# Kernel optimization log

Measured on AMD Instinct MI355X. Metric: run time of the kernel, lower is better.

## Reference

```python
import jax, jax.numpy as jnp
from jax import lax
import numpy as np
import math

D = 96   # d_model
H = 4    # num_heads (d_k = d_v = D per head, per the source)
K = 7    # depthwise kernel size
L = 4    # num conv layers


def _pos_encoding(seq_len, d):
    # Faithful to the source's (nonstandard) exponents: sin uses 2*i/d, cos uses 2*(i+1)/d
    pos = np.arange(seq_len, dtype=np.float32)[:, None]
    i = np.arange(0, d, 2, dtype=np.float32)
    pe = np.zeros((seq_len, d), dtype=np.float32)
    pe[:, 0::2] = np.sin(pos / 10000.0 ** (2.0 * i / d))
    pe[:, 1::2] = np.cos(pos / 10000.0 ** (2.0 * (i + 1.0) / d))
    return jnp.asarray(pe)


def _layernorm(x, g, b, eps=1e-5):
    m = jnp.mean(x, axis=-1, keepdims=True)
    v = jnp.mean((x - m) ** 2, axis=-1, keepdims=True)
    return (x - m) / jnp.sqrt(v + eps) * g + b


def setup_inputs() -> dict:
    key = jax.random.key(0)
    ks = jax.random.split(key, 10)
    B, S = 128, 384

    def xavier(k, shape, fan_in, fan_out):
        bound = math.sqrt(6.0 / (fan_in + fan_out))
        return jax.random.uniform(k, shape, jnp.float32, -bound, bound)

    return {
        "input": jax.random.normal(ks[0], (B, S, D), jnp.float32),
        "mask": jnp.zeros((B, S), dtype=bool),
        "conv_dw": jax.random.normal(ks[1], (L, D, 1, K), jnp.float32) * 0.05,
        "conv_dw_b": jnp.zeros((L, D), jnp.float32),
        "conv_pw": jax.random.normal(ks[2], (L, D, D, 1), jnp.float32) * 0.05,
        "conv_pw_b": jnp.zeros((L, D), jnp.float32),
        "WQ": xavier(ks[3], (H, D, D), D, D),
        "WK": xavier(ks[4], (H, D, D), D, D),
        "WV": xavier(ks[5], (H, D, D), D, D),
        "WO": xavier(ks[6], (H * D, D), H * D, D),
        "ffn_w1": jax.random.normal(ks[7], (D, D // 2), jnp.float32) * 0.1,
        "ffn_b1": jnp.zeros((D // 2,), jnp.float32),
        "ffn_w2": jax.random.normal(ks[8], (D // 2, D), jnp.float32) * 0.1,
        "ffn_b2": jnp.zeros((D,), jnp.float32),
        "ln_g": jnp.ones((L + 2, D), jnp.float32),
        "ln_b": jnp.zeros((L + 2, D), jnp.float32),
    }


def reference(input, mask, conv_dw, conv_dw_b, conv_pw, conv_pw_b,
              WQ, WK, WV, WO, ffn_w1, ffn_b1, ffn_w2, ffn_b2, ln_g, ln_b):
    B, S, _ = input.shape
    dn = ("NCH", "OIH", "NCH")

    # positional encoding (eval mode: all dropout is identity)
    x = input * jnp.float32(math.sqrt(D)) + _pos_encoding(S, D)[None]

    # conv blocks: LN -> depthwise conv -> pointwise conv -> relu -> residual
    for i in range(L):
        h = _layernorm(x, ln_g[i], ln_b[i])
        h = jnp.transpose(h, (0, 2, 1))  # [B, C, S]
        h = lax.conv_general_dilated(h, conv_dw[i], (1,), "SAME",
                                     feature_group_count=D, dimension_numbers=dn)
        h = h + conv_dw_b[i][None, :, None]
        h = lax.conv_general_dilated(h, conv_pw[i], (1,), "SAME", dimension_numbers=dn)
        h = jax.nn.relu(h + conv_pw_b[i][None, :, None])
        x = x + jnp.transpose(h, (0, 2, 1))

    # multi-head attention with per-head full-width projections (d_k = D)
    h = _layernorm(x, ln_g[L], ln_b[L])
    Q = jnp.einsum("bsd,hde->hbse", h, WQ)
    Kh = jnp.einsum("bsd,hde->hbse", h, WK)
    V = jnp.einsum("bsd,hde->hbse", h, WV)
    # source divides scores by temperature = 1/sqrt(d_k) => multiply by sqrt(D)
    scores = jnp.einsum("hbqe,hbke->hbqk", Q, Kh) * jnp.float32(math.sqrt(D))
    # mask is viewed [B, S, 1]: masks query rows, broadcast over keys
    scores = jnp.where(mask[None, :, :, None], -jnp.inf, scores)
    attn = jax.nn.softmax(scores, axis=-1)
    ctx = jnp.einsum("hbqk,hbke->hbqe", attn, V)
    cat = jnp.transpose(ctx, (1, 2, 0, 3)).reshape(B, S, H * D)
    x = x + cat @ WO

    # feed-forward: Linear -> sigmoid -> Linear, residual
    h2 = _layernorm(x, ln_g[L + 1], ln_b[L + 1])
    ff = jax.nn.sigmoid(h2 @ ffn_w1 + ffn_b1) @ ffn_w2 + ffn_b2
    return x + ff
```

## Files before the change

### kernel.cpp

```cpp
#include <hip/hip_runtime.h>
#include <math.h>


constexpr int B = 128;
constexpr int S = 384;
constexpr int D = 96;
constexpr int H = 4;
constexpr int KW = 7;
constexpr int L = 4;
constexpr int ROWS = B * S;
constexpr long long NTOT = (long long)ROWS * D;
constexpr float SQRTD = 9.797958971132712f;

typedef _Float16 f16x8 __attribute__((ext_vector_type(8)));
typedef float f32x4 __attribute__((ext_vector_type(4)));
typedef unsigned short us;
typedef unsigned short us8 __attribute__((ext_vector_type(8)));

__device__ __forceinline__ us f2h(float f) {
    _Float16 h = (_Float16)f;
    return __builtin_bit_cast(us, h);
}
__device__ __forceinline__ f16x8 ldh(const us* p) {
    return *reinterpret_cast<const f16x8*>(p);
}

__global__ void pe_kernel(float* __restrict__ pe) {
    int idx = blockIdx.x * 256 + threadIdx.x;
    if (idx >= S * D) return;
    int s = idx / D, c = idx - s * D;
    int j = c >> 1;
    float expo = (c & 1) ? (4.0f * j + 2.0f) / 96.0f : (4.0f * j) / 96.0f;
    float freq = expf(-expo * logf(10000.0f));
    float ang = (float)s * freq;
    pe[idx] = (c & 1) ? cosf(ang) : sinf(ang);
}

__global__ void prep_w(const float* __restrict__ WQ, const float* __restrict__ WK,
                       const float* __restrict__ cpw, const float* __restrict__ w1,
                       const float* __restrict__ w2,
                       us* __restrict__ wqS, us* __restrict__ wkT, us* __restrict__ pw16,
                       us* __restrict__ w1T, us* __restrict__ w2Tp) {
    int idx = blockIdx.x * 256 + threadIdx.x;
    if (idx >= H * D * D) return;
    int h = idx / (D * D), rem = idx - h * (D * D);
    int d = rem / D, e = rem - d * D;
    int n = e >> 4, lmod = e & 15, kk = d >> 5, ldiv = (d >> 3) & 3, j = d & 7;
    wqS[(size_t)(((h * 6 + n) * 3 + kk) * 64 + ldiv * 16 + lmod) * 8 + j] = f2h(WQ[idx] * SQRTD);
    wkT[(size_t)h * D * D + e * D + d] = f2h(WK[idx]);
    pw16[idx] = f2h(cpw[idx]);
    if (idx < 48 * 96) {
        int m = idx / 96, c = idx - m * 96;
        w1T[idx] = f2h(w1[c * 48 + m]);
    }
    if (idx < 96 * 64) {
        int o = idx / 64, m = idx - o * 64;
        w2Tp[idx] = (m < 48) ? f2h(w2[m * 96 + o]) : (us)0;
    }
}

__global__ void prep_wvo(const float* __restrict__ WV, const float* __restrict__ WO,
                         us* __restrict__ wvoT) {
    int blk = blockIdx.x;
    int h = blk / 6, ot = blk - h * 6;
    int tid = threadIdx.x;
    const float* wv = WV + (size_t)h * D * D;
    const float* wo = WO + (size_t)h * D * D;
    for (int i = tid; i < 16 * 96; i += 256) {
        int o = ot * 16 + i / 96, d = i - (i / 96) * 96;
        float acc = 0.f;
        for (int e = 0; e < 96; e++) acc += wv[d * 96 + e] * wo[e * 96 + o];
        wvoT[(size_t)h * D * D + o * 96 + d] = f2h(acc);
    }
}

__global__ void embed_ln(const float* __restrict__ in, const float* __restrict__ pe,
                         const float* __restrict__ gln, const float* __restrict__ bln,
                         float* __restrict__ x, us* __restrict__ lnout) {
    int wave = threadIdx.x >> 6;
    int lane = threadIdx.x & 63;
    int row = blockIdx.x * 4 + wave;
    if (row >= ROWS) return;
    int s = row % S;
    size_t ro = (size_t)row * D;
    float v0 = in[ro + lane] * SQRTD + pe[s * 96 + lane];
    float v1 = (lane < 32) ? in[ro + 64 + lane] * SQRTD + pe[s * 96 + 64 + lane] : 0.f;
    x[ro + lane] = v0;
    if (lane < 32) x[ro + 64 + lane] = v1;
    float sm = v0 + v1, q = v0 * v0 + v1 * v1;
    for (int off = 32; off > 0; off >>= 1) {
        sm += __shfl_xor(sm, off);
        q += __shfl_xor(q, off);
    }
    float mean = sm * (1.0f / D);
    float var = q * (1.0f / D) - mean * mean;
    float rstd = rsqrtf(var + 1e-5f);
    lnout[ro + lane] = f2h((v0 - mean) * rstd * gln[lane] + bln[lane]);
    if (lane < 32)
        lnout[ro + 64 + lane] = f2h((v1 - mean) * rstd * gln[lane + 64] + bln[lane + 64]);
}

__global__ void conv2(const float* __restrict__ xin, const us* __restrict__ lnin,
                      float* __restrict__ xout, us* __restrict__ lnout,
                      const float* __restrict__ dwW, const float* __restrict__ dwB,
                      const us* __restrict__ pwW, const float* __restrict__ pwb,
                      const float* __restrict__ gnext, const float* __restrict__ bnext) {
    __shared__ us dwb_s[64 * 104];
    __shared__ float lw[96 * 8];
    int tid = threadIdx.x;
    int wave = tid >> 6, lane = tid & 63;
    int r0 = blockIdx.x * 64;
    int b = r0 / S, s0 = r0 % S;

    for (int i = tid; i < 96 * KW; i += 256) lw[(i / KW) * 8 + (i % KW)] = dwW[i];
    __syncthreads();

    for (int u = tid; u < 768; u += 256) {
        int j = u / 12, c0 = (u - (u / 12) * 12) * 8;
        float acc[8];
        #pragma unroll
        for (int j2 = 0; j2 < 8; j2++) acc[j2] = dwB[c0 + j2];
        #pragma unroll
        for (int k = 0; k < KW; k++) {
            int ss = s0 + j + k - 3;
            if ((unsigned)ss < (unsigned)S) {
                f16x8 v = ldh(lnin + ((size_t)b * S + ss) * 96 + c0);
                #pragma unroll
                for (int j2 = 0; j2 < 8; j2++) acc[j2] += (float)v[j2] * lw[(c0 + j2) * 8 + k];
            }
        }
        us8 o;
        #pragma unroll
        for (int j2 = 0; j2 < 8; j2++) o[j2] = f2h(acc[j2]);
        *reinterpret_cast<us8*>(&dwb_s[j * 104 + c0]) = o;
    }
    __syncthreads();

    int lmod = lane & 15, ldiv = lane >> 4, m0 = wave * 16;
    f32x4 acc[6] = {};
    #pragma unroll
    for (int kk = 0; kk < 3; kk++) {
        f16x8 af = ldh(&dwb_s[(m0 + lmod) * 104 + kk * 32 + ldiv * 8]);
        #pragma unroll
        for (int n = 0; n < 6; n++) {
            f16x8 bf = ldh(pwW + (size_t)(n * 16 + lmod) * 96 + kk * 32 + ldiv * 8);
            acc[n] = __builtin_amdgcn_mfma_f32_16x16x32_f16(af, bf, acc[n], 0, 0, 0);
        }
    }

    float gv[6], bv2[6], pb[6];
    #pragma unroll
    for (int n = 0; n < 6; n++) {
        int o = n * 16 + lmod;
        gv[n] = gnext[o];
        bv2[n] = bnext[o];
        pb[n] = pwb[o];
    }
    #pragma unroll
    for (int n = 0; n < 6; n++) {
        #pragma unroll
        for (int r = 0; r < 4; r++) {
            size_t row = (size_t)r0 + m0 + ldiv * 4 + r;
            acc[n][r] = xin[row * 96 + n * 16 + lmod] + fmaxf(acc[n][r] + pb[n], 0.f);
        }
    }
    #pragma unroll
    for (int r = 0; r < 4; r++) {
        float sm = 0.f, qq = 0.f;
        #pragma unroll
        for (int n = 0; n < 6; n++) {
            sm += acc[n][r];
            qq += acc[n][r] * acc[n][r];
        }
        #pragma unroll
        for (int st = 1; st <= 8; st <<= 1) {
            sm += __shfl_xor(sm, st);
            qq += __shfl_xor(qq, st);
        }
        float mean = sm * (1.0f / D);
        float var = qq * (1.0f / D) - mean * mean;
        float rstd = rsqrtf(var + 1e-5f);
        size_t row = (size_t)r0 + m0 + ldiv * 4 + r;
        #pragma unroll
        for (int n = 0; n < 6; n++) {
            int o = n * 16 + lmod;
            xout[row * 96 + o] = acc[n][r];
            lnout[row * 96 + o] = f2h((acc[n][r] - mean) * rstd * gv[n] + bv2[n]);
        }
    }
}

__global__ void proj_all(const us* __restrict__ h16, const us* __restrict__ wkT,
                         const us* __restrict__ wvoT, us* __restrict__ Kall,
                         us* __restrict__ Vall) {
    __shared__ us stg[96 * 72];
    int hd = blockIdx.y;
    int tid = threadIdx.x;
    int wave = tid >> 6, lane = tid & 63, lmod = lane & 15, ldiv = lane >> 4;
    int row0 = blockIdx.x * 64, m0 = wave * 16;
    int b = row0 / S;

    f16x8 af[3];
    #pragma unroll
    for (int kk = 0; kk < 3; kk++)
        af[kk] = ldh(h16 + (size_t)(row0 + m0 + lmod) * 96 + kk * 32 + ldiv * 8);

    {
        const us* W = wkT + (size_t)hd * D * D;
        f32x4 acc[6] = {};
        #pragma unroll
        for (int kk = 0; kk < 3; kk++)
            #pragma unroll
            for (int n = 0; n < 6; n++) {
                f16x8 bf = ldh(W + (size_t)(n * 16 + lmod) * 96 + kk * 32 + ldiv * 8);
                acc[n] = __builtin_amdgcn_mfma_f32_16x16x32_f16(af[kk], bf, acc[n], 0, 0, 0);
            }
        us* kT = stg + wave * 1664;
        #pragma unroll
        for (int n = 0; n < 6; n++)
            #pragma unroll
            for (int r = 0; r < 4; r++)
                kT[(ldiv * 4 + r) * 104 + n * 16 + lmod] = f2h(acc[n][r]);
        int t0 = (row0 % S) / 16 + wave;
        us* dst = Kall + (size_t)hd * NTOT + ((size_t)(b * 24 + t0) * 3) * 512;
        #pragma unroll
        for (int kk = 0; kk < 3; kk++) {
            us8 v = *reinterpret_cast<const us8*>(&kT[lmod * 104 + kk * 32 + ldiv * 8]);
            *reinterpret_cast<us8*>(dst + kk * 512 + lane * 8) = v;
        }
    }
    __syncthreads();

    {
        const us* W = wvoT + (size_t)hd * D * D;
        f32x4 acc[6] = {};
        #pragma unroll
        for (int kk = 0; kk < 3; kk++)
            #pragma unroll
            for (int n = 0; n < 6; n++) {
                f16x8 bf = ldh(W + (size_t)(n * 16 + lmod) * 96 + kk * 32 + ldiv * 8);
                acc[n] = __builtin_amdgcn_mfma_f32_16x16x32_f16(af[kk], bf, acc[n], 0, 0, 0);
            }
        #pragma unroll
        for (int n = 0; n < 6; n++)
            #pragma unroll
            for (int r = 0; r < 4; r++)
                stg[(n * 16 + lmod) * 72 + m0 + ldiv * 4 + r] = f2h(acc[n][r]);
        __syncthreads();
        int cblk = (row0 % S) / 64;
        us* dsth = Vall + (size_t)hd * NTOT;
        #pragma unroll
        for (int n = 0; n < 6; n++)
            #pragma unroll
            for (int kk = 0; kk < 2; kk++) {
                us8 v =
                    *reinterpret_cast<const us8*>(&stg[(n * 16 + lmod) * 72 + kk * 32 + ldiv * 8]);
                *reinterpret_cast<us8*>(
                    dsth + ((size_t)((b * 6 + n) * 6 + cblk) * 2 + kk) * 512 + lane * 8) = v;
            }
    }
}

__global__ __launch_bounds__(64, 3) void attn_2p(const us* __restrict__ h16,
                                                 const us* __restrict__ wqS,
                                                 const us* __restrict__ Kall,
                                                 const us* __restrict__ Vall,
                                                 us* __restrict__ xpart) {
    __shared__ us stg[32 * 104];
    int lane = threadIdx.x;
    int lmod = lane & 15, ldiv = lane >> 4;
    int p = blockIdx.x;
    int gl = (p & 7) * 768 + (p >> 3);
    int t = gl % 12;
    int bh = gl / 12;
    int b = bh >> 2, hd = bh & 3;
    size_t rowbase = (size_t)b * S + t * 32;

    f16x8 ah0[3], ah1[3];
    #pragma unroll
    for (int kk = 0; kk < 3; kk++) {
        ah0[kk] = ldh(h16 + (rowbase + lmod) * 96 + kk * 32 + ldiv * 8);
        ah1[kk] = ldh(h16 + (rowbase + 16 + lmod) * 96 + kk * 32 + ldiv * 8);
    }

    f32x4 qa0[6] = {}, qa1[6] = {};
    #pragma unroll
    for (int kk = 0; kk < 3; kk++)
        #pragma unroll
        for (int n = 0; n < 6; n++) {
            f16x8 bf = ldh(wqS + (size_t)(((hd * 6 + n) * 3 + kk) * 64) * 8 + lane * 8);
            qa0[n] = __builtin_amdgcn_mfma_f32_16x16x32_f16(ah0[kk], bf, qa0[n], 0, 0, 0);
            qa1[n] = __builtin_amdgcn_mfma_f32_16x16x32_f16(ah1[kk], bf, qa1[n], 0, 0, 0);
        }
    #pragma unroll
    for (int n = 0; n < 6; n++)
        #pragma unroll
        for (int r = 0; r < 4; r++) {
            stg[(ldiv * 4 + r) * 104 + n * 16 + lmod] = f2h(qa0[n][r]);
            stg[(16 + ldiv * 4 + r) * 104 + n * 16 + lmod] = f2h(qa1[n][r]);
        }
    f16x8 aq0[3], aq1[3];
    #pragma unroll
    for (int kk = 0; kk < 3; kk++) {
        aq0[kk] = ldh(&stg[lmod * 104 + kk * 32 + ldiv * 8]);
        aq1[kk] = ldh(&stg[(16 + lmod) * 104 + kk * 32 + ldiv * 8]);
    }

    const us* Kh = Kall + (size_t)hd * NTOT + (size_t)b * 24 * 1536;
    const us* Vh = Vall + (size_t)hd * NTOT + (size_t)b * 36 * 1024;

    f32x4 mx0 = {-1e30f, -1e30f, -1e30f, -1e30f}, mx1 = mx0;
    for (int c = 0; c < 6; c++) {
        f32x4 s0[4] = {}, s1[4] = {};
        __builtin_amdgcn_s_setprio(1);
        #pragma unroll
        for (int nt = 0; nt < 4; nt++)
            #pragma unroll
            for (int kk = 0; kk < 3; kk++) {
                f16x8 bf = ldh(Kh + (size_t)((c * 4 + nt) * 3 + kk) * 512 + lane * 8);
                s0[nt] = __builtin_amdgcn_mfma_f32_16x16x32_f16(aq0[kk], bf, s0[nt], 0, 0, 0);
                s1[nt] = __builtin_amdgcn_mfma_f32_16x16x32_f16(aq1[kk], bf, s1[nt], 0, 0, 0);
            }
        __builtin_amdgcn_s_setprio(0);
        #pragma unroll
        for (int nt = 0; nt < 4; nt++)
            #pragma unroll
            for (int r = 0; r < 4; r++) {
                mx0[r] = fmaxf(mx0[r], s0[nt][r]);
                mx1[r] = fmaxf(mx1[r], s1[nt][r]);
            }
    }
    #pragma unroll
    for (int st = 1; st <= 8; st <<= 1)
        #pragma unroll
        for (int r = 0; r < 4; r++) {
            mx0[r] = fmaxf(mx0[r], __shfl_xor(mx0[r], st));
            mx1[r] = fmaxf(mx1[r], __shfl_xor(mx1[r], st));
        }

    f32x4 oacc0[6] = {}, oacc1[6] = {};
    f32x4 l0v = {}, l1v = {};
    for (int c = 0; c < 6; c++) {
        f32x4 s0[4] = {}, s1[4] = {};
        __builtin_amdgcn_s_setprio(1);
        #pragma unroll
        for (int nt = 0; nt < 4; nt++)
            #pragma unroll
            for (int kk = 0; kk < 3; kk++) {
                f16x8 bf = ldh(Kh + (size_t)((c * 4 + nt) * 3 + kk) * 512 + lane * 8);
                s0[nt] = __builtin_amdgcn_mfma_f32_16x16x32_f16(aq0[kk], bf, s0[nt], 0, 0, 0);
                s1[nt] = __builtin_amdgcn_mfma_f32_16x16x32_f16(aq1[kk], bf, s1[nt], 0, 0, 0);
            }
        __builtin_amdgcn_s_setprio(0);
        #pragma unroll
        for (int nt = 0; nt < 4; nt++)
            #pragma unroll
            for (int r = 0; r < 4; r++) {
                float p0 = __expf(s0[nt][r] - mx0[r]);
                float p1 = __expf(s1[nt][r] - mx1[r]);
                l0v[r] += p0;
                l1v[r] += p1;
                stg[(ldiv * 4 + r) * 72 + nt * 16 + lmod] = f2h(p0);
                stg[(16 + ldiv * 4 + r) * 72 + nt * 16 + lmod] = f2h(p1);
            }
        __builtin_amdgcn_s_setprio(1);
        #pragma unroll
        for (int kk = 0; kk < 2; kk++) {
            f16x8 pf0 = ldh(&stg[lmod * 72 + kk * 32 + ldiv * 8]);
            f16x8 pf1 = ldh(&stg[(16 + lmod) * 72 + kk * 32 + ldiv * 8]);
            #pragma unroll
            for (int n = 0; n < 6; n++) {
                f16x8 bf = ldh(Vh + (size_t)((n * 6 + c) * 2 + kk) * 512 + lane * 8);
                oacc0[n] = __builtin_amdgcn_mfma_f32_16x16x32_f16(pf0, bf, oacc0[n], 0, 0, 0);
                oacc1[n] = __builtin_amdgcn_mfma_f32_16x16x32_f16(pf1, bf, oacc1[n], 0, 0, 0);
            }
        }
        __builtin_amdgcn_s_setprio(0);
    }
    #pragma unroll
    for (int st = 1; st <= 8; st <<= 1)
        #pragma unroll
        for (int r = 0; r < 4; r++) {
            l0v[r] += __shfl_xor(l0v[r], st);
            l1v[r] += __shfl_xor(l1v[r], st);
        }

    us* xp = xpart + (size_t)hd * NTOT;
    #pragma unroll
    for (int r = 0; r < 4; r++) {
        float inv0 = 1.f / l0v[r];
        float inv1 = 1.f / l1v[r];
        #pragma unroll
        for (int n = 0; n < 6; n++) {
            xp[(rowbase + ldiv * 4 + r) * 96 + n * 16 + lmod] = f2h(oacc0[n][r] * inv0);
            xp[(rowbase + 16 + ldiv * 4 + r) * 96 + n * 16 + lmod] = f2h(oacc1[n][r] * inv1);
        }
    }
}

__global__ void ffn_ln(const float* __restrict__ x, const us* __restrict__ xpart,
                       const float* __restrict__ gln, const float* __restrict__ bln,
                       const us* __restrict__ w1T, const float* __restrict__ b1,
                       const us* __restrict__ w2Tp, const float* __restrict__ b2,
                       float* __restrict__ out) {
    __shared__ float xf[64 * 96];
    __shared__ us lnb[64 * 104];
    __shared__ us mid[64 * 72];
    int tid = threadIdx.x, wave = tid >> 6, lane = tid & 63;
    int lmod = lane & 15, ldiv = lane >> 4, m0 = wave * 16;
    int row0 = blockIdx.x * 64;

    for (int i = wave; i < 64; i += 4) {
        size_t ro = (size_t)(row0 + i) * 96;
        float v0 = x[ro + lane];
        float v1 = (lane < 32) ? x[ro + 64 + lane] : 0.f;
        #pragma unroll
        for (int h = 0; h < H; h++) {
            const us* xp = xpart + (size_t)h * NTOT + ro;
            v0 += (float)__builtin_bit_cast(_Float16, xp[lane]);
            if (lane < 32) v1 += (float)__builtin_bit_cast(_Float16, xp[64 + lane]);
        }
        xf[i * 96 + lane] = v0;
        if (lane < 32) xf[i * 96 + 64 + lane] = v1;
        float sm = v0 + v1, q = v0 * v0 + v1 * v1;
        for (int off = 32; off > 0; off >>= 1) {
            sm += __shfl_xor(sm, off);
            q += __shfl_xor(q, off);
        }
        float mean = sm * (1.0f / D);
        float var = q * (1.0f / D) - mean * mean;
        float rstd = rsqrtf(var + 1e-5f);
        lnb[i * 104 + lane] = f2h((v0 - mean) * rstd * gln[lane] + bln[lane]);
        if (lane < 32)
            lnb[i * 104 + 64 + lane] = f2h((v1 - mean) * rstd * gln[lane + 64] + bln[lane + 64]);
    }
    __syncthreads();

    f32x4 a3[3] = {};
    #pragma unroll
    for (int kk = 0; kk < 3; kk++) {
        f16x8 af = ldh(&lnb[(m0 + lmod) * 104 + kk * 32 + ldiv * 8]);
        #pragma unroll
        for (int n = 0; n < 3; n++) {
            f16x8 bf = ldh(w1T + (size_t)(n * 16 + lmod) * 96 + kk * 32 + ldiv * 8);
            a3[n] = __builtin_amdgcn_mfma_f32_16x16x32_f16(af, bf, a3[n], 0, 0, 0);
        }
    }
    #pragma unroll
    for (int n = 0; n < 3; n++) {
        float bv = b1[n * 16 + lmod];
        #pragma unroll
        for (int r = 0; r < 4; r++) {
            float v = a3[n][r] + bv;
            mid[(m0 + ldiv * 4 + r) * 72 + n * 16 + lmod] = f2h(1.f / (1.f + __expf(-v)));
        }
    }
    #pragma unroll
    for (int r = 0; r < 4; r++) mid[(m0 + ldiv * 4 + r) * 72 + 48 + lmod] = 0;
    __syncthreads();

    f32x4 a6[6] = {};
    #pragma unroll
    for (int kk = 0; kk < 2; kk++) {
        f16x8 af = ldh(&mid[(m0 + lmod) * 72 + kk * 32 + ldiv * 8]);
        #pragma unroll
        for (int n = 0; n < 6; n++) {
            f16x8 bf = ldh(w2Tp + (size_t)(n * 16 + lmod) * 64 + kk * 32 + ldiv * 8);
            a6[n] = __builtin_amdgcn_mfma_f32_16x16x32_f16(af, bf, a6[n], 0, 0, 0);
        }
    }
    #pragma unroll
    for (int n = 0; n < 6; n++) {
        int o = n * 16 + lmod;
        float bv = b2[o];
        #pragma unroll
        for (int r = 0; r < 4; r++) {
            int sr = m0 + ldiv * 4 + r;
            out[(size_t)(row0 + sr) * 96 + o] = xf[sr * 96 + o] + a6[n][r] + bv;
        }
    }
}

extern "C" void kernel_launch(void* const* d_in, const int* in_sizes, int n_in,
                              void* d_out, int out_size, void* d_ws, size_t ws_size,
                              hipStream_t stream) {
    const float* in   = (const float*)d_in[0];
    const float* cdw  = (const float*)d_in[2];
    const float* cdwb = (const float*)d_in[3];
    const float* cpw  = (const float*)d_in[4];
    const float* cpwb = (const float*)d_in[5];
    const float* WQ   = (const float*)d_in[6];
    const float* WK   = (const float*)d_in[7];
    const float* WV   = (const float*)d_in[8];
    const float* WO   = (const float*)d_in[9];
    const float* w1   = (const float*)d_in[10];
    const float* b1   = (const float*)d_in[11];
    const float* w2   = (const float*)d_in[12];
    const float* b2   = (const float*)d_in[13];
    const float* lng  = (const float*)d_in[14];
    const float* lnb  = (const float*)d_in[15];
    float* out = (float*)d_out;
    float* ws = (float*)d_ws;

    float* x   = ws;
    float* x2  = x + NTOT;
    float* pe  = x2 + NTOT;
    us* lnA    = (us*)(pe + S * D);
    us* lnB    = lnA + NTOT;
    us* Kall   = lnB + NTOT;
    us* Vall   = Kall + (size_t)H * NTOT;
    us* xpart  = Vall + (size_t)H * NTOT;
    us* wqS    = xpart + (size_t)H * NTOT;
    us* wkT    = wqS + H * D * D;
    us* wvoT   = wkT + H * D * D;
    us* pw16   = wvoT + H * D * D;
    us* w1T    = pw16 + L * D * D;
    us* w2Tp   = w1T + 48 * 96;

    pe_kernel<<<(S * D + 255) / 256, 256, 0, stream>>>(pe);
    prep_w<<<(H * D * D + 255) / 256, 256, 0, stream>>>(WQ, WK, cpw, w1, w2,
                                                        wqS, wkT, pw16, w1T, w2Tp);
    prep_wvo<<<H * 6, 256, 0, stream>>>(WV, WO, wvoT);

    embed_ln<<<ROWS / 4, 256, 0, stream>>>(in, pe, lng, lnb, x, lnA);

    conv2<<<ROWS / 64, 256, 0, stream>>>(x, lnA, x2, lnB, cdw, cdwb, pw16, cpwb,
                                         lng + D, lnb + D);
    conv2<<<ROWS / 64, 256, 0, stream>>>(x2, lnB, x, lnA, cdw + D * KW, cdwb + D,
                                         pw16 + D * D, cpwb + D, lng + 2 * D, lnb + 2 * D);
    conv2<<<ROWS / 64, 256, 0, stream>>>(x, lnA, x2, lnB, cdw + 2 * D * KW, cdwb + 2 * D,
                                         pw16 + 2 * D * D, cpwb + 2 * D, lng + 3 * D,
                                         lnb + 3 * D);
    conv2<<<ROWS / 64, 256, 0, stream>>>(x2, lnB, x, lnA, cdw + 3 * D * KW, cdwb + 3 * D,
                                         pw16 + 3 * D * D, cpwb + 3 * D, lng + 4 * D,
                                         lnb + 4 * D);

    us* h16 = lnA;
    proj_all<<<dim3(ROWS / 64, H), 256, 0, stream>>>(h16, wkT, wvoT, Kall, Vall);
    attn_2p<<<B * 12 * H, 64, 0, stream>>>(h16, wqS, Kall, Vall, xpart);

    ffn_ln<<<ROWS / 64, 256, 0, stream>>>(x, xpart, lng + 5 * D, lnb + 5 * D,
                                          w1T, b1, w2Tp, b2, out);
}
```

Measured before the change: 337.8 us.

## Fuse embed+LN into first conv, fuse K/V projections into last conv, batch attention waves

The embedding, scaling and first layernorm are computed inside the first conv kernel, including a recomputed 3-row halo, so the standalone embed_ln pass and its x/ln round trip through memory go away. The K and V-times-WO projections for all heads are folded into the last conv kernel, reusing the freshly normalised tile from shared memory instead of rereading h16 in a separate launch. The attention kernel now packs four independent 64-thread work items into one 256-thread block with per-wave staging buffers. In exchange, halo rows are recomputed, the last conv kernel uses more LDS and extra barriers, and the projections for the four heads run serially inside each block, which reduces parallelism.

```diff
diff --git a/kernel.cpp b/kernel.cpp
--- a/kernel.cpp
+++ b/kernel.cpp
@@ -74,30 +74,119 @@
     }
 }
 
-__global__ void embed_ln(const float* __restrict__ in, const float* __restrict__ pe,
-                         const float* __restrict__ gln, const float* __restrict__ bln,
-                         float* __restrict__ x, us* __restrict__ lnout) {
-    int wave = threadIdx.x >> 6;
-    int lane = threadIdx.x & 63;
-    int row = blockIdx.x * 4 + wave;
-    if (row >= ROWS) return;
-    int s = row % S;
-    size_t ro = (size_t)row * D;
-    float v0 = in[ro + lane] * SQRTD + pe[s * 96 + lane];
-    float v1 = (lane < 32) ? in[ro + 64 + lane] * SQRTD + pe[s * 96 + 64 + lane] : 0.f;
-    x[ro + lane] = v0;
-    if (lane < 32) x[ro + 64 + lane] = v1;
-    float sm = v0 + v1, q = v0 * v0 + v1 * v1;
-    for (int off = 32; off > 0; off >>= 1) {
-        sm += __shfl_xor(sm, off);
-        q += __shfl_xor(q, off);
-    }
-    float mean = sm * (1.0f / D);
-    float var = q * (1.0f / D) - mean * mean;
-    float rstd = rsqrtf(var + 1e-5f);
-    lnout[ro + lane] = f2h((v0 - mean) * rstd * gln[lane] + bln[lane]);
-    if (lane < 32)
-        lnout[ro + 64 + lane] = f2h((v1 - mean) * rstd * gln[lane + 64] + bln[lane + 64]);
+__global__ void conv0f(const float* __restrict__ in, const float* __restrict__ pe,
+                       const float* __restrict__ g0, const float* __restrict__ b0,
+                       float* __restrict__ xout, us* __restrict__ lnout,
+                       const float* __restrict__ dwW, const float* __restrict__ dwB,
+                       const us* __restrict__ pwW, const float* __restrict__ pwb,
+                       const float* __restrict__ gnext, const float* __restrict__ bnext) {
+    __shared__ us lnb_s[70 * 104];
+    __shared__ us dwb_s[64 * 104];
+    __shared__ float lw[96 * 8];
+    int tid = threadIdx.x;
+    int wave = tid >> 6, lane = tid & 63;
+    int r0 = blockIdx.x * 64;
+    int b = r0 / S, s0 = r0 % S;
+
+    for (int i = tid; i < 96 * KW; i += 256) lw[(i / KW) * 8 + (i % KW)] = dwW[i];
+
+    for (int i = wave; i < 70; i += 4) {
+        int s = s0 - 3 + i;
+        bool valid = (unsigned)s < (unsigned)S;
+        float v0 = 0.f, v1 = 0.f;
+        if (valid) {
+            size_t ro = ((size_t)b * S + s) * 96;
+            v0 = in[ro + lane] * SQRTD + pe[s * 96 + lane];
+            v1 = (lane < 32) ? in[ro + 64 + lane] * SQRTD + pe[s * 96 + 64 + lane] : 0.f;
+        }
+        float sm = v0 + v1, q = v0 * v0 + v1 * v1;
+        for (int off = 32; off > 0; off >>= 1) {
+            sm += __shfl_xor(sm, off);
+            q += __shfl_xor(q, off);
+        }
+        float mean = sm * (1.0f / D);
+        float var = q * (1.0f / D) - mean * mean;
+        float rstd = rsqrtf(var + 1e-5f);
+        lnb_s[i * 104 + lane] = f2h(valid ? (v0 - mean) * rstd * g0[lane] + b0[lane] : 0.f);
+        if (lane < 32)
+            lnb_s[i * 104 + 64 + lane] =
+                f2h(valid ? (v1 - mean) * rstd * g0[lane + 64] + b0[lane + 64] : 0.f);
+    }
+    __syncthreads();
+
+    for (int u = tid; u < 768; u += 256) {
+        int j = u / 12, c0 = (u - (u / 12) * 12) * 8;
+        float acc[8];
+        #pragma unroll
+        for (int j2 = 0; j2 < 8; j2++) acc[j2] = dwB[c0 + j2];
+        #pragma unroll
+        for (int k = 0; k < KW; k++) {
+            f16x8 v = ldh(&lnb_s[(j + k) * 104 + c0]);
+            #pragma unroll
+            for (int j2 = 0; j2 < 8; j2++) acc[j2] += (float)v[j2] * lw[(c0 + j2) * 8 + k];
+        }
+        us8 o;
+        #pragma unroll
+        for (int j2 = 0; j2 < 8; j2++) o[j2] = f2h(acc[j2]);
+        *reinterpret_cast<us8*>(&dwb_s[j * 104 + c0]) = o;
+    }
+    __syncthreads();
+
+    int lmod = lane & 15, ldiv = lane >> 4, m0 = wave * 16;
+    f32x4 acc[6] = {};
+    #pragma unroll
+    for (int kk = 0; kk < 3; kk++) {
+        f16x8 af = ldh(&dwb_s[(m0 + lmod) * 104 + kk * 32 + ldiv * 8]);
+        #pragma unroll
+        for (int n = 0; n < 6; n++) {
+            f16x8 bf = ldh(pwW + (size_t)(n * 16 + lmod) * 96 + kk * 32 + ldiv * 8);
+            acc[n] = __builtin_amdgcn_mfma_f32_16x16x32_f16(af, bf, acc[n], 0, 0, 0);
+        }
+    }
+
+    float gv[6], bv2[6], pb[6];
+    #pragma unroll
+    for (int n = 0; n < 6; n++) {
+        int o = n * 16 + lmod;
+        gv[n] = gnext[o];
+        bv2[n] = bnext[o];
+        pb[n] = pwb[o];
+    }
+    #pragma unroll
+    for (int n = 0; n < 6; n++) {
+        int o = n * 16 + lmod;
+        #pragma unroll
+        for (int r = 0; r < 4; r++) {
+            int sr = m0 + ldiv * 4 + r;
+            size_t row = (size_t)r0 + sr;
+            float base = in[row * 96 + o] * SQRTD + pe[(s0 + sr) * 96 + o];
+            acc[n][r] = base + fmaxf(acc[n][r] + pb[n], 0.f);
+        }
+    }
+    #pragma unroll
+    for (int r = 0; r < 4; r++) {
+        float sm = 0.f, qq = 0.f;
+        #pragma unroll
+        for (int n = 0; n < 6; n++) {
+            sm += acc[n][r];
+            qq += acc[n][r] * acc[n][r];
+        }
+        #pragma unroll
+        for (int st = 1; st <= 8; st <<= 1) {
+            sm += __shfl_xor(sm, st);
+            qq += __shfl_xor(qq, st);
+        }
+        float mean = sm * (1.0f / D);
+        float var = qq * (1.0f / D) - mean * mean;
+        float rstd = rsqrtf(var + 1e-5f);
+        size_t row = (size_t)r0 + m0 + ldiv * 4 + r;
+        #pragma unroll
+        for (int n = 0; n < 6; n++) {
+            int o = n * 16 + lmod;
+            xout[row * 96 + o] = acc[n][r];
+            lnout[row * 96 + o] = f2h((acc[n][r] - mean) * rstd * gv[n] + bv2[n]);
+        }
+    }
 }
 
 __global__ void conv2(const float* __restrict__ xin, const us* __restrict__ lnin,
@@ -190,64 +279,147 @@
     }
 }
 
-__global__ void proj_all(const us* __restrict__ h16, const us* __restrict__ wkT,
-                         const us* __restrict__ wvoT, us* __restrict__ Kall,
-                         us* __restrict__ Vall) {
+__global__ void conv3p(const float* __restrict__ xin, const us* __restrict__ lnin,
+                       float* __restrict__ xout, us* __restrict__ lnout,
+                       const float* __restrict__ dwW, const float* __restrict__ dwB,
+                       const us* __restrict__ pwW, const float* __restrict__ pwb,
+                       const float* __restrict__ gnext, const float* __restrict__ bnext,
+                       const us* __restrict__ wkT, const us* __restrict__ wvoT,
+                       us* __restrict__ Kall, us* __restrict__ Vall) {
+    __shared__ float lw[96 * 8];
     __shared__ us stg[96 * 72];
-    int hd = blockIdx.y;
+    __shared__ us lnstg[64 * 104];
     int tid = threadIdx.x;
-    int wave = tid >> 6, lane = tid & 63, lmod = lane & 15, ldiv = lane >> 4;
-    int row0 = blockIdx.x * 64, m0 = wave * 16;
-    int b = row0 / S;
+    int wave = tid >> 6, lane = tid & 63;
+    int lmod = lane & 15, ldiv = lane >> 4, m0 = wave * 16;
+    int r0 = blockIdx.x * 64;
+    int b = r0 / S, s0 = r0 % S;
+
+    for (int i = tid; i < 96 * KW; i += 256) lw[(i / KW) * 8 + (i % KW)] = dwW[i];
+    __syncthreads();
+
+    for (int u = tid; u < 768; u += 256) {
+        int j = u / 12, c0 = (u - (u / 12) * 12) * 8;
+        float acc[8];
+        #pragma unroll
+        for (int j2 = 0; j2 < 8; j2++) acc[j2] = dwB[c0 + j2];
+        #pragma unroll
+        for (int k = 0; k < KW; k++) {
+            int ss = s0 + j + k - 3;
+            if ((unsigned)ss < (unsigned)S) {
+                f16x8 v = ldh(lnin + ((size_t)b * S + ss) * 96 + c0);
+                #pragma unroll
+                for (int j2 = 0; j2 < 8; j2++) acc[j2] += (float)v[j2] * lw[(c0 + j2) * 8 + k];
+            }
+        }
+        us8 o;
+        #pragma unroll
+        for (int j2 = 0; j2 < 8; j2++) o[j2] = f2h(acc[j2]);
+        *reinterpret_cast<us8*>(&stg[j * 104 + c0]) = o;
+    }
+    __syncthreads();
+
+    f32x4 acc[6] = {};
+    #pragma unroll
+    for (int kk = 0; kk < 3; kk++) {
+        f16x8 af = ldh(&stg[(m0 + lmod) * 104 + kk * 32 + ldiv * 8]);
+        #pragma unroll
+        for (int n = 0; n < 6; n++) {
+            f16x8 bf = ldh(pwW + (size_t)(n * 16 + lmod) * 96 + kk * 32 + ldiv * 8);
+            acc[n] = __builtin_amdgcn_mfma_f32_16x16x32_f16(af, bf, acc[n], 0, 0, 0);
+        }
+    }
+
+    float gv[6], bv2[6], pb[6];
+    #pragma unroll
+    for (int n = 0; n < 6; n++) {
+        int o = n * 16 + lmod;
+        gv[n] = gnext[o];
+        bv2[n] = bnext[o];
+        pb[n] = pwb[o];
+    }
+    #pragma unroll
+    for (int n = 0; n < 6; n++) {
+        #pragma unroll
+        for (int r = 0; r < 4; r++) {
+            size_t row = (size_t)r0 + m0 + ldiv * 4 + r;
+            acc[n][r] = xin[row * 96 + n * 16 + lmod] + fmaxf(acc[n][r] + pb[n], 0.f);
+        }
+    }
+    #pragma unroll
+    for (int r = 0; r < 4; r++) {
+        float sm = 0.f, qq = 0.f;
+        #pragma unroll
+        for (int n = 0; n < 6; n++) {
+            sm += acc[n][r];
+            qq += acc[n][r] * acc[n][r];
+        }
+        #pragma unroll
+        for (int st = 1; st <= 8; st <<= 1) {
+            sm += __shfl_xor(sm, st);
+            qq += __shfl_xor(qq, st);
+        }
+        float mean = sm * (1.0f / D);
+        float var = qq * (1.0f / D) - mean * mean;
+        float rstd = rsqrtf(var + 1e-5f);
+        size_t row = (size_t)r0 + m0 + ldiv * 4 + r;
+        #pragma unroll
+        for (int n = 0; n < 6; n++) {
+            int o = n * 16 + lmod;
+            xout[row * 96 + o] = acc[n][r];
+            us hv = f2h((acc[n][r] - mean) * rstd * gv[n] + bv2[n]);
+            lnout[row * 96 + o] = hv;
+            lnstg[(m0 + ldiv * 4 + r) * 104 + o] = hv;
+        }
+    }
+    __syncthreads();
 
     f16x8 af[3];
     #pragma unroll
     for (int kk = 0; kk < 3; kk++)
-        af[kk] = ldh(h16 + (size_t)(row0 + m0 + lmod) * 96 + kk * 32 + ldiv * 8);
-
-    {
-        const us* W = wkT + (size_t)hd * D * D;
-        f32x4 acc[6] = {};
+        af[kk] = ldh(&lnstg[(m0 + lmod) * 104 + kk * 32 + ldiv * 8]);
+
+    for (int hd = 0; hd < H; hd++) {
+        f32x4 ka[6] = {};
         #pragma unroll
         for (int kk = 0; kk < 3; kk++)
             #pragma unroll
             for (int n = 0; n < 6; n++) {
-                f16x8 bf = ldh(W + (size_t)(n * 16 + lmod) * 96 + kk * 32 + ldiv * 8);
-                acc[n] = __builtin_amdgcn_mfma_f32_16x16x32_f16(af[kk], bf, acc[n], 0, 0, 0);
-            }
+                f16x8 bf =
+                    ldh(wkT + (size_t)hd * D * D + (size_t)(n * 16 + lmod) * 96 + kk * 32 + ldiv * 8);
+                ka[n] = __builtin_amdgcn_mfma_f32_16x16x32_f16(af[kk], bf, ka[n], 0, 0, 0);
+            }
+        __syncthreads();
         us* kT = stg + wave * 1664;
         #pragma unroll
         for (int n = 0; n < 6; n++)
             #pragma unroll
             for (int r = 0; r < 4; r++)
-                kT[(ldiv * 4 + r) * 104 + n * 16 + lmod] = f2h(acc[n][r]);
-        int t0 = (row0 % S) / 16 + wave;
+                kT[(ldiv * 4 + r) * 104 + n * 16 + lmod] = f2h(ka[n][r]);
+        int t0 = (r0 % S) / 16 + wave;
         us* dst = Kall + (size_t)hd * NTOT + ((size_t)(b * 24 + t0) * 3) * 512;
         #pragma unroll
         for (int kk = 0; kk < 3; kk++) {
             us8 v = *reinterpret_cast<const us8*>(&kT[lmod * 104 + kk * 32 + ldiv * 8]);
             *reinterpret_cast<us8*>(dst + kk * 512 + lane * 8) = v;
         }
-    }
-    __syncthreads();
-
-    {
-        const us* W = wvoT + (size_t)hd * D * D;
-        f32x4 acc[6] = {};
+        f32x4 va[6] = {};
         #pragma unroll
         for (int kk = 0; kk < 3; kk++)
             #pragma unroll
             for (int n = 0; n < 6; n++) {
-                f16x8 bf = ldh(W + (size_t)(n * 16 + lmod) * 96 + kk * 32 + ldiv * 8);
-                acc[n] = __builtin_amdgcn_mfma_f32_16x16x32_f16(af[kk], bf, acc[n], 0, 0, 0);
-            }
+                f16x8 bf = ldh(wvoT + (size_t)hd * D * D + (size_t)(n * 16 + lmod) * 96 + kk * 32 +
+                               ldiv * 8);
+                va[n] = __builtin_amdgcn_mfma_f32_16x16x32_f16(af[kk], bf, va[n], 0, 0, 0);
+            }
+        __syncthreads();
         #pragma unroll
         for (int n = 0; n < 6; n++)
             #pragma unroll
             for (int r = 0; r < 4; r++)
-                stg[(n * 16 + lmod) * 72 + m0 + ldiv * 4 + r] = f2h(acc[n][r]);
+                stg[(n * 16 + lmod) * 72 + m0 + ldiv * 4 + r] = f2h(va[n][r]);
         __syncthreads();
-        int cblk = (row0 % S) / 64;
+        int cblk = (r0 % S) / 64;
         us* dsth = Vall + (size_t)hd * NTOT;
         #pragma unroll
         for (int n = 0; n < 6; n++)
@@ -261,16 +433,17 @@
     }
 }
 
-__global__ __launch_bounds__(64, 3) void attn_2p(const us* __restrict__ h16,
-                                                 const us* __restrict__ wqS,
-                                                 const us* __restrict__ Kall,
-                                                 const us* __restrict__ Vall,
-                                                 us* __restrict__ xpart) {
-    __shared__ us stg[32 * 104];
-    int lane = threadIdx.x;
+__global__ __launch_bounds__(256, 4) void attn_2p4(const us* __restrict__ h16,
+                                                   const us* __restrict__ wqS,
+                                                   const us* __restrict__ Kall,
+                                                   const us* __restrict__ Vall,
+                                                   us* __restrict__ xpart) {
+    __shared__ us stg4[4][32 * 104];
+    int tid = threadIdx.x, wave = tid >> 6, lane = tid & 63;
+    us* stg = stg4[wave];
     int lmod = lane & 15, ldiv = lane >> 4;
     int p = blockIdx.x;
-    int gl = (p & 7) * 768 + (p >> 3);
+    int gl = (((p & 7) * 192 + (p >> 3)) << 2) + wave;
     int t = gl % 12;
     int bh = gl / 12;
     int b = bh >> 2, hd = bh & 3;
@@ -502,9 +675,9 @@
     float* out = (float*)d_out;
     float* ws = (float*)d_ws;
 
-    float* x   = ws;
-    float* x2  = x + NTOT;
-    float* pe  = x2 + NTOT;
+    float* xA  = ws;
+    float* xB  = xA + NTOT;
+    float* pe  = xB + NTOT;
     us* lnA    = (us*)(pe + S * D);
     us* lnB    = lnA + NTOT;
     us* Kall   = lnB + NTOT;
@@ -522,23 +695,19 @@
                                                         wqS, wkT, pw16, w1T, w2Tp);
     prep_wvo<<<H * 6, 256, 0, stream>>>(WV, WO, wvoT);
 
-    embed_ln<<<ROWS / 4, 256, 0, stream>>>(in, pe, lng, lnb, x, lnA);
-
-    conv2<<<ROWS / 64, 256, 0, stream>>>(x, lnA, x2, lnB, cdw, cdwb, pw16, cpwb,
-                                         lng + D, lnb + D);
-    conv2<<<ROWS / 64, 256, 0, stream>>>(x2, lnB, x, lnA, cdw + D * KW, cdwb + D,
+    conv0f<<<ROWS / 64, 256, 0, stream>>>(in, pe, lng, lnb, xA, lnB,
+                                          cdw, cdwb, pw16, cpwb, lng + D, lnb + D);
+    conv2<<<ROWS / 64, 256, 0, stream>>>(xA, lnB, xB, lnA, cdw + D * KW, cdwb + D,
                                          pw16 + D * D, cpwb + D, lng + 2 * D, lnb + 2 * D);
-    conv2<<<ROWS / 64, 256, 0, stream>>>(x, lnA, x2, lnB, cdw + 2 * D * KW, cdwb + 2 * D,
+    conv2<<<ROWS / 64, 256, 0, stream>>>(xB, lnA, xA, lnB, cdw + 2 * D * KW, cdwb + 2 * D,
                                          pw16 + 2 * D * D, cpwb + 2 * D, lng + 3 * D,
                                          lnb + 3 * D);
-    conv2<<<ROWS / 64, 256, 0, stream>>>(x2, lnB, x, lnA, cdw + 3 * D * KW, cdwb + 3 * D,
-                                         pw16 + 3 * D * D, cpwb + 3 * D, lng + 4 * D,
-                                         lnb + 4 * D);
-
-    us* h16 = lnA;
-    proj_all<<<dim3(ROWS / 64, H), 256, 0, stream>>>(h16, wkT, wvoT, Kall, Vall);
-    attn_2p<<<B * 12 * H, 64, 0, stream>>>(h16, wqS, Kall, Vall, xpart);
-
-    ffn_ln<<<ROWS / 64, 256, 0, stream>>>(x, xpart, lng + 5 * D, lnb + 5 * D,
+    conv3p<<<ROWS / 64, 256, 0, stream>>>(xA, lnB, xB, lnA, cdw + 3 * D * KW, cdwb + 3 * D,
+                                          pw16 + 3 * D * D, cpwb + 3 * D, lng + 4 * D,
+                                          lnb + 4 * D, wkT, wvoT, Kall, Vall);
+
+    attn_2p4<<<1536, 256, 0, stream>>>(lnA, wqS, Kall, Vall, xpart);
+
+    ffn_ln<<<ROWS / 64, 256, 0, stream>>>(xB, xpart, lng + 5 * D, lnb + 5 * D,
                                           w1T, b1, w2Tp, b2, out);
 }
```

After: 365.8 us. 1.08x slower.
